# Kernel optimization log

Hardware: AMD Instinct MI355X
Metric: run time of the kernel (lower is better)

The kernel has to match this reference:

```python
import jax, jax.numpy as jnp
import numpy as np

NUM_HEADS = 16


def setup_inputs() -> dict:
    key = jax.random.key(0)
    ks = jax.random.split(key, 4)
    B, S, D = 2, 2048, 1024
    scale = 1.0 / np.sqrt(D)
    x = jax.random.normal(ks[0], (B, S, D), dtype=jnp.float32)
    Wq = jax.random.normal(ks[1], (D, D), dtype=jnp.float32) * scale
    Wk = jax.random.normal(ks[2], (D, D), dtype=jnp.float32) * scale
    Wv = jax.random.normal(ks[3], (D, D), dtype=jnp.float32) * scale
    bq = jnp.zeros((D,), dtype=jnp.float32)
    bk = jnp.zeros((D,), dtype=jnp.float32)
    bv = jnp.zeros((D,), dtype=jnp.float32)
    return {"x": x, "Wq": Wq, "bq": bq, "Wk": Wk, "bk": bk, "Wv": Wv, "bv": bv}


def _split_heads(t, H):
    B, S, D = t.shape
    return t.reshape(B, S, H, D // H).transpose(0, 2, 1, 3)  # (B,H,S,depth)


def reference(x, Wq, bq, Wk, bk, Wv, bv):
    H = NUM_HEADS
    B, S, D = x.shape
    depth = D // H
    q = _split_heads(x @ Wq + bq, H)
    k = _split_heads(x @ Wk + bk, H)
    v = _split_heads(x @ Wv + bv, H)
    # causal mask: strictly-upper-triangular ones, added as finfo.min * mask
    mask = 1.0 - jnp.tril(jnp.ones((S, S), dtype=jnp.float32))
    scores = jnp.einsum("bhqd,bhkd->bhqk", q, k) / jnp.sqrt(jnp.float32(depth))
    scores = scores + jnp.float32(np.finfo(np.float32).min) * mask
    probs = jax.nn.softmax(scores, axis=-1)
    att = jnp.einsum("bhqk,bhkd->bhqd", probs, v)
    return att.transpose(0, 2, 1, 3).reshape(B, S, D)
```

## Files before the change

### kernel.cpp

```cpp
#include <hip/hip_runtime.h>
#include <hip/hip_bf16.h>

#define B_ 2
#define S_ 2048
#define D_ 1024
#define H_ 16
#define DH 64
#define M_ (B_*S_)
#define NT_ (S_/64)

using bf16x8 = __attribute__((ext_vector_type(8))) __bf16;
using f32x4  = __attribute__((ext_vector_type(4))) float;

__device__ __forceinline__ int swz(int row) { return ((row ^ (row >> 3)) & 7) << 3; }

__device__ __forceinline__ void glds16(const __bf16* g, __bf16* l) {
#if __has_builtin(__builtin_amdgcn_global_load_lds)
  __builtin_amdgcn_global_load_lds(
      (const __attribute__((address_space(1))) unsigned int*)g,
      (__attribute__((address_space(3))) unsigned int*)l, 16, 0, 0);
#else
  *(bf16x8*)l = *(const bf16x8*)g;
#endif
}

__global__ __launch_bounds__(256) void conv_x(const float* __restrict__ x,
                                              __bf16* __restrict__ xb) {
  int idx = blockIdx.x * 256 + threadIdx.x;
  int m = idx >> 7, k = (idx & 127) * 8;
  float4 a = *(const float4*)&x[(size_t)m * D_ + k];
  float4 b = *(const float4*)&x[(size_t)m * D_ + k + 4];
  bf16x8 o;
  o[0]=(__bf16)a.x; o[1]=(__bf16)a.y; o[2]=(__bf16)a.z; o[3]=(__bf16)a.w;
  o[4]=(__bf16)b.x; o[5]=(__bf16)b.y; o[6]=(__bf16)b.z; o[7]=(__bf16)b.w;
  *(bf16x8*)&xb[(size_t)m * D_ + (k & ~63) + ((k & 63) ^ swz(m))] = o;
}

__global__ __launch_bounds__(256) void conv_w(const float* __restrict__ Wq,
                                              const float* __restrict__ Wk,
                                              const float* __restrict__ Wv,
                                              __bf16* __restrict__ wt) {
  int z = blockIdx.z;
  const float* __restrict__ W = (z == 0) ? Wq : (z == 1) ? Wk : Wv;
  __bf16* __restrict__ Wt = wt + (size_t)z * D_ * D_;
  __shared__ __bf16 Lt[64 * 66];
  int tid = threadIdx.x;
  int k0 = blockIdx.x * 64, n0 = blockIdx.y * 64;
  #pragma unroll
  for (int i = 0; i < 4; ++i) {
    int f4 = i * 256 + tid;
    int r = f4 >> 4, c4 = (f4 & 15) * 4;
    float4 v = *(const float4*)&W[(size_t)(k0 + r) * D_ + n0 + c4];
    Lt[(c4 + 0) * 66 + r] = (__bf16)v.x;
    Lt[(c4 + 1) * 66 + r] = (__bf16)v.y;
    Lt[(c4 + 2) * 66 + r] = (__bf16)v.z;
    Lt[(c4 + 3) * 66 + r] = (__bf16)v.w;
  }
  __syncthreads();
  #pragma unroll
  for (int i = 0; i < 2; ++i) {
    int idx = i * 256 + tid;
    int n = idx >> 3, kc = (idx & 7) * 8;
    int nf = n0 + n;
    bf16x8 o;
    #pragma unroll
    for (int j = 0; j < 8; ++j) o[j] = Lt[n * 66 + kc + j];
    *(bf16x8*)&Wt[(size_t)nf * D_ + k0 + (kc ^ swz(nf))] = o;
  }
}

#define BM 256
#define BN 256
#define BK 64
#define NKT (D_/BK)

__global__ __launch_bounds__(512, 2) void qkv_gemm(
    const __bf16* __restrict__ xb, const __bf16* __restrict__ wt,
    const float* __restrict__ bq, const float* __restrict__ bk,
    const float* __restrict__ bv, __bf16* __restrict__ qkv) {
  int z = blockIdx.z;
  const __bf16* __restrict__ Wt = wt + (size_t)z * D_ * D_;
  const float* __restrict__ bias = (z == 0) ? bq : (z == 1) ? bk : bv;
  __bf16* __restrict__ out = qkv + (size_t)z * M_ * D_;
  const float scale = (z == 0) ? 0.125f : 1.0f;

  __shared__ __bf16 Al[2][BM * BK];
  __shared__ __bf16 Bl[2][BM * BK];

  int tid = threadIdx.x, lane = tid & 63, w = tid >> 6;
  int m0 = blockIdx.y * BM, n0 = blockIdx.x * BN;
  int wr = (w >> 2) * 128;
  int wc = (w & 3) * 64;

  f32x4 acc[8][4] = {};

#define STAGE(buf, kt)                                                        \
  {                                                                           \
    int k0 = (kt) * BK;                                                       \
    _Pragma("unroll")                                                         \
    for (int r = 0; r < 4; ++r) {                                             \
      int e = (r * 512 + tid) * 8;                                            \
      int row = e >> 6, col = e & 63;                                         \
      glds16(&xb[(size_t)(m0 + row) * D_ + k0 + col], &Al[buf][e]);           \
      glds16(&Wt[(size_t)(n0 + row) * D_ + k0 + col], &Bl[buf][e]);           \
    }                                                                         \
  }

  STAGE(0, 0);
  __syncthreads();

  int cur = 0;
  for (int kt = 0; kt < NKT; ++kt) {
    if (kt + 1 < NKT) STAGE(cur ^ 1, kt + 1);
    #pragma unroll
    for (int kk = 0; kk < 2; ++kk) {
      bf16x8 af[8], bfr[4];
      #pragma unroll
      for (int mi = 0; mi < 8; ++mi) {
        int row = wr + mi * 16 + (lane & 15);
        af[mi] = *(const bf16x8*)&Al[cur][row * 64 +
                 ((kk * 32 + (lane >> 4) * 8) ^ swz(row))];
      }
      #pragma unroll
      for (int ni = 0; ni < 4; ++ni) {
        int col = wc + ni * 16 + (lane & 15);
        bfr[ni] = *(const bf16x8*)&Bl[cur][col * 64 +
                  ((kk * 32 + (lane >> 4) * 8) ^ swz(col))];
      }
      #pragma unroll
      for (int mi = 0; mi < 8; ++mi)
        #pragma unroll
        for (int ni = 0; ni < 4; ++ni)
          acc[mi][ni] = __builtin_amdgcn_mfma_f32_16x16x32_bf16(
              af[mi], bfr[ni], acc[mi][ni], 0, 0, 0);
    }
    __syncthreads();
    cur ^= 1;
  }
#undef STAGE

  #pragma unroll
  for (int mi = 0; mi < 8; ++mi) {
    #pragma unroll
    for (int ni = 0; ni < 4; ++ni) {
      int col = n0 + wc + ni * 16 + (lane & 15);
      int h = col >> 6, dh = col & 63;
      float bv_ = bias[col];
      #pragma unroll
      for (int r = 0; r < 4; ++r) {
        int row = m0 + wr + mi * 16 + (lane >> 4) * 4 + r;
        int b = row >> 11, s = row & 2047;
        out[((size_t)(b * H_ + h) * S_ + s) * DH + dh] =
            (__bf16)((acc[mi][ni][r] + bv_) * scale);
      }
    }
  }
}

__device__ __forceinline__ void attn_tile(
    const bf16x8* aq, f32x4* accO, float* mrow, float* lrow,
    const __bf16* __restrict__ Kl, const __bf16* __restrict__ Vt,
    __bf16* __restrict__ Plw, int lane, int kv0, int qbase, int diag) {
  f32x4 sf[4];
  __builtin_amdgcn_s_setprio(1);
  #pragma unroll
  for (int f = 0; f < 4; ++f) {
    f32x4 zz = {};
    int col = f * 16 + (lane & 15);
    int sc = swz(col);
    #pragma unroll
    for (int kk = 0; kk < 2; ++kk) {
      bf16x8 bk = *(const bf16x8*)&Kl[col * 64 + ((kk * 32 + (lane >> 4) * 8) ^ sc)];
      zz = __builtin_amdgcn_mfma_f32_16x16x32_bf16(aq[kk], bk, zz, 0, 0, 0);
    }
    sf[f] = zz;
  }
  __builtin_amdgcn_s_setprio(0);

  if (diag) {
    #pragma unroll
    for (int f = 0; f < 4; ++f) {
      int kvg = kv0 + f * 16 + (lane & 15);
      #pragma unroll
      for (int r = 0; r < 4; ++r) {
        int qg = qbase + (lane >> 4) * 4 + r;
        if (kvg > qg) sf[f][r] = -1e30f;
      }
    }
  }

  float alpha[4];
  #pragma unroll
  for (int r = 0; r < 4; ++r) {
    float mx = fmaxf(fmaxf(sf[0][r], sf[1][r]), fmaxf(sf[2][r], sf[3][r]));
    #pragma unroll
    for (int off = 8; off >= 1; off >>= 1)
      mx = fmaxf(mx, __shfl_xor(mx, off, 64));
    float mnew = fmaxf(mrow[r], mx);
    alpha[r] = __expf(mrow[r] - mnew);
    mrow[r] = mnew;
    float rs = 0.f;
    #pragma unroll
    for (int f = 0; f < 4; ++f) {
      float p = __expf(sf[f][r] - mnew);
      sf[f][r] = p;
      rs += p;
    }
    #pragma unroll
    for (int off = 8; off >= 1; off >>= 1)
      rs += __shfl_xor(rs, off, 64);
    lrow[r] = lrow[r] * alpha[r] + rs;
  }

  #pragma unroll
  for (int f = 0; f < 4; ++f)
    #pragma unroll
    for (int r = 0; r < 4; ++r) {
      int row = (lane >> 4) * 4 + r;
      Plw[row * 64 + ((f * 16 + (lane & 15)) ^ swz(row))] = (__bf16)sf[f][r];
    }

  #pragma unroll
  for (int f = 0; f < 4; ++f)
    #pragma unroll
    for (int r = 0; r < 4; ++r)
      accO[f][r] *= alpha[r];

  __builtin_amdgcn_s_setprio(1);
  #pragma unroll
  for (int kk = 0; kk < 2; ++kk) {
    int prow = lane & 15;
    bf16x8 pa = *(const bf16x8*)&Plw[prow * 64 + ((kk * 32 + (lane >> 4) * 8) ^ swz(prow))];
    #pragma unroll
    for (int f = 0; f < 4; ++f) {
      int vrow = f * 16 + (lane & 15);
      bf16x8 vb = *(const bf16x8*)&Vt[vrow * 64 + ((kk * 32 + (lane >> 4) * 8) ^ swz(vrow))];
      accO[f] = __builtin_amdgcn_mfma_f32_16x16x32_bf16(pa, vb, accO[f], 0, 0, 0);
    }
  }
  __builtin_amdgcn_s_setprio(0);
}

__device__ __forceinline__ void attn_out(
    const f32x4* accO, const float* lrow, float* __restrict__ out,
    int b, int h, int qbase, int lane) {
  #pragma unroll
  for (int f = 0; f < 4; ++f) {
    int dh = f * 16 + (lane & 15);
    #pragma unroll
    for (int r = 0; r < 4; ++r) {
      int qg = qbase + (lane >> 4) * 4 + r;
      out[((size_t)(b * S_ + qg)) * D_ + h * DH + dh] = accO[f][r] / lrow[r];
    }
  }
}

__global__ __launch_bounds__(256) void attn(
    const __bf16* __restrict__ Q, const __bf16* __restrict__ K,
    const __bf16* __restrict__ V, float* __restrict__ out) {
  __shared__ __bf16 Kl[64 * 64];
  __shared__ __bf16 Vt[64 * 64];
  __shared__ __bf16 Pl[4][16 * 64];

  int tid = threadIdx.x, lane = tid & 63, w = tid >> 6;
  int bx = blockIdx.x, h = blockIdx.y, b = blockIdx.z;
  int qA0 = bx * 64, qB0 = (NT_ - 1 - bx) * 64;
  size_t base = ((size_t)(b * H_ + h)) * S_ * DH;
  const __bf16* __restrict__ Qg = Q + base;
  const __bf16* __restrict__ Kg = K + base;
  const __bf16* __restrict__ Vg = V + base;

  bf16x8 aqA[2], aqB[2];
  int qra = qA0 + w * 16 + (lane & 15), qrb = qB0 + w * 16 + (lane & 15);
  #pragma unroll
  for (int kk = 0; kk < 2; ++kk) {
    aqA[kk] = *(const bf16x8*)&Qg[(size_t)qra * DH + kk * 32 + (lane >> 4) * 8];
    aqB[kk] = *(const bf16x8*)&Qg[(size_t)qrb * DH + kk * 32 + (lane >> 4) * 8];
  }

  f32x4 accA[4] = {}, accB[4] = {};
  float mA[4], lA[4], mB[4], lB[4];
  #pragma unroll
  for (int r = 0; r < 4; ++r) { mA[r] = mB[r] = -1e30f; lA[r] = lB[r] = 0.f; }

  const int ktA = bx, ktB = NT_ - 1 - bx;
  for (int kt = 0; kt <= ktB; ++kt) {
    int kv0 = kt * 64;
    #pragma unroll
    for (int i = 0; i < 2; ++i) {
      int e = (i * 256 + tid) * 8;
      int kv = e >> 6, d0 = e & 63;
      bf16x8 k8 = *(const bf16x8*)&Kg[(size_t)(kv0 + kv) * DH + d0];
      *(bf16x8*)&Kl[kv * 64 + (d0 ^ swz(kv))] = k8;
      bf16x8 v8 = *(const bf16x8*)&Vg[(size_t)(kv0 + kv) * DH + d0];
      #pragma unroll
      for (int j = 0; j < 8; ++j) {
        int row = d0 + j;
        Vt[row * 64 + (kv ^ swz(row))] = v8[j];
      }
    }
    __syncthreads();

    attn_tile(aqB, accB, mB, lB, Kl, Vt, Pl[w], lane, kv0, qB0 + w * 16, kt == ktB);
    if (kt <= ktA)
      attn_tile(aqA, accA, mA, lA, Kl, Vt, Pl[w], lane, kv0, qA0 + w * 16, kt == ktA);
    __syncthreads();
  }

  attn_out(accA, lA, out, b, h, qA0 + w * 16, lane);
  attn_out(accB, lB, out, b, h, qB0 + w * 16, lane);
}

extern "C" void kernel_launch(void* const* d_in, const int* in_sizes, int n_in,
                              void* d_out, int out_size, void* d_ws, size_t ws_size,
                              hipStream_t stream) {
  const float* x  = (const float*)d_in[0];
  const float* Wq = (const float*)d_in[1];
  const float* bq = (const float*)d_in[2];
  const float* Wk = (const float*)d_in[3];
  const float* bk = (const float*)d_in[4];
  const float* Wv = (const float*)d_in[5];
  const float* bv = (const float*)d_in[6];
  float* out = (float*)d_out;

  __bf16* xb  = (__bf16*)d_ws;
  __bf16* wt  = xb + (size_t)M_ * D_;
  __bf16* qkv = wt + (size_t)3 * D_ * D_;
  __bf16* wsq = qkv;
  __bf16* wsk = qkv + (size_t)M_ * D_;
  __bf16* wsv = qkv + (size_t)2 * M_ * D_;

  conv_x<<<(M_ * (D_ / 8)) / 256, 256, 0, stream>>>(x, xb);
  conv_w<<<dim3(D_ / 64, D_ / 64, 3), 256, 0, stream>>>(Wq, Wk, Wv, wt);
  qkv_gemm<<<dim3(D_ / BN, M_ / BM, 3), 512, 0, stream>>>(xb, wt, bq, bk, bv, qkv);
  attn<<<dim3(NT_ / 2, H_, B_), 256, 0, stream>>>(wsq, wsk, wsv, out);
}
```

Before: 198.9 us.

## Pre-transpose V, register-prefetch K/V tiles, and compute transposed scores in attention

Adds a separate kernel that transposes V into a per-head (DH x S) layout in reused workspace, so the attention kernel can stage V with vector stores instead of scalar transposing stores. The attention loop now prefetches the next K/V tile into registers while computing the current one. QK^T is computed transposed so each lane owns one query row, which cuts the softmax shuffles and holds m/l as scalars. Launch bounds change too: the GEMM drops its min-blocks hint and attention asks for 4 blocks per CU. The cost is an extra launch and extra register pressure from the prefetch buffers.

```diff
diff --git a/kernel.cpp b/kernel.cpp
--- a/kernel.cpp
+++ b/kernel.cpp
@@ -74,7 +74,7 @@
 #define BK 64
 #define NKT (D_/BK)
 
-__global__ __launch_bounds__(512, 2) void qkv_gemm(
+__global__ __launch_bounds__(512) void qkv_gemm(
     const __bf16* __restrict__ xb, const __bf16* __restrict__ wt,
     const float* __restrict__ bq, const float* __restrict__ bk,
     const float* __restrict__ bv, __bf16* __restrict__ qkv) {
@@ -157,107 +157,138 @@
   }
 }
 
-__device__ __forceinline__ void attn_tile(
-    const bf16x8* aq, f32x4* accO, float* mrow, float* lrow,
+__global__ __launch_bounds__(256) void vtrans(const __bf16* __restrict__ v,
+                                              __bf16* __restrict__ vt) {
+  __shared__ __bf16 Lt[64 * 64];
+  int tid = threadIdx.x;
+  int s0 = blockIdx.x * 64;
+  int h = blockIdx.y, b = blockIdx.z;
+  const __bf16* __restrict__ src = v + ((size_t)(b * H_ + h)) * S_ * DH;
+  __bf16* __restrict__ dst = vt + ((size_t)(b * H_ + h)) * DH * S_;
+  #pragma unroll
+  for (int i = 0; i < 2; ++i) {
+    int e = (i * 256 + tid) * 8;
+    int s = e >> 6, d0 = e & 63;
+    bf16x8 r = *(const bf16x8*)&src[(size_t)(s0 + s) * DH + d0];
+    #pragma unroll
+    for (int j = 0; j < 8; ++j) {
+      int d = d0 + j;
+      Lt[d * 64 + (s ^ swz(d))] = r[j];
+    }
+  }
+  __syncthreads();
+  #pragma unroll
+  for (int i = 0; i < 2; ++i) {
+    int e = (i * 256 + tid) * 8;
+    int d = e >> 6, sc = e & 63;
+    bf16x8 o = *(const bf16x8*)&Lt[d * 64 + (sc ^ swz(d))];
+    *(bf16x8*)&dst[(size_t)d * S_ + s0 + sc] = o;
+  }
+}
+
+__device__ __forceinline__ void attn_tile_sw(
+    const bf16x8* aq, f32x4* accO, float& m_reg, float& l_reg,
     const __bf16* __restrict__ Kl, const __bf16* __restrict__ Vt,
-    __bf16* __restrict__ Plw, int lane, int kv0, int qbase, int diag) {
-  f32x4 sf[4];
+    __bf16* __restrict__ Plw, int lane, int kv0, int qbase, bool diag) {
+  const int g = lane >> 4;
+  const int ql = lane & 15;
+  f32x4 sfT[4];
   __builtin_amdgcn_s_setprio(1);
   #pragma unroll
   for (int f = 0; f < 4; ++f) {
     f32x4 zz = {};
-    int col = f * 16 + (lane & 15);
-    int sc = swz(col);
+    int row = f * 16 + ql;
+    int sr = swz(row);
     #pragma unroll
     for (int kk = 0; kk < 2; ++kk) {
-      bf16x8 bk = *(const bf16x8*)&Kl[col * 64 + ((kk * 32 + (lane >> 4) * 8) ^ sc)];
-      zz = __builtin_amdgcn_mfma_f32_16x16x32_bf16(aq[kk], bk, zz, 0, 0, 0);
-    }
-    sf[f] = zz;
+      bf16x8 ka = *(const bf16x8*)&Kl[row * 64 + ((kk * 32 + g * 8) ^ sr)];
+      zz = __builtin_amdgcn_mfma_f32_16x16x32_bf16(ka, aq[kk], zz, 0, 0, 0);
+    }
+    sfT[f] = zz;
   }
   __builtin_amdgcn_s_setprio(0);
 
   if (diag) {
+    int qg = qbase + ql;
+    #pragma unroll
+    for (int f = 0; f < 4; ++f)
+      #pragma unroll
+      for (int r = 0; r < 4; ++r)
+        if (kv0 + f * 16 + g * 4 + r > qg) sfT[f][r] = -1e30f;
+  }
+
+  float mx = sfT[0][0];
+  #pragma unroll
+  for (int f = 0; f < 4; ++f)
+    #pragma unroll
+    for (int r = 0; r < 4; ++r) mx = fmaxf(mx, sfT[f][r]);
+  mx = fmaxf(mx, __shfl_xor(mx, 16, 64));
+  mx = fmaxf(mx, __shfl_xor(mx, 32, 64));
+  float mnew = fmaxf(m_reg, mx);
+  float alpha = __expf(m_reg - mnew);
+  m_reg = mnew;
+  float rs = 0.f;
+  #pragma unroll
+  for (int f = 0; f < 4; ++f)
+    #pragma unroll
+    for (int r = 0; r < 4; ++r) {
+      float p = __expf(sfT[f][r] - mnew);
+      sfT[f][r] = p;
+      rs += p;
+    }
+  rs += __shfl_xor(rs, 16, 64);
+  rs += __shfl_xor(rs, 32, 64);
+  l_reg = l_reg * alpha + rs;
+
+  const int key = (ql & 7) << 3;
+  #pragma unroll
+  for (int f = 0; f < 4; ++f)
+    #pragma unroll
+    for (int r = 0; r < 4; ++r)
+      Plw[ql * 64 + ((f * 16 + g * 4 + r) ^ key)] = (__bf16)sfT[f][r];
+
+  float ab[4];
+  #pragma unroll
+  for (int r = 0; r < 4; ++r) ab[r] = __shfl(alpha, g * 4 + r, 16);
+  #pragma unroll
+  for (int f = 0; f < 4; ++f)
+    #pragma unroll
+    for (int r = 0; r < 4; ++r) accO[f][r] *= ab[r];
+
+  __builtin_amdgcn_s_setprio(1);
+  #pragma unroll
+  for (int kk = 0; kk < 2; ++kk) {
+    bf16x8 pa = *(const bf16x8*)&Plw[ql * 64 + ((kk * 32 + g * 8) ^ key)];
     #pragma unroll
     for (int f = 0; f < 4; ++f) {
-      int kvg = kv0 + f * 16 + (lane & 15);
-      #pragma unroll
-      for (int r = 0; r < 4; ++r) {
-        int qg = qbase + (lane >> 4) * 4 + r;
-        if (kvg > qg) sf[f][r] = -1e30f;
-      }
-    }
-  }
-
-  float alpha[4];
-  #pragma unroll
-  for (int r = 0; r < 4; ++r) {
-    float mx = fmaxf(fmaxf(sf[0][r], sf[1][r]), fmaxf(sf[2][r], sf[3][r]));
-    #pragma unroll
-    for (int off = 8; off >= 1; off >>= 1)
-      mx = fmaxf(mx, __shfl_xor(mx, off, 64));
-    float mnew = fmaxf(mrow[r], mx);
-    alpha[r] = __expf(mrow[r] - mnew);
-    mrow[r] = mnew;
-    float rs = 0.f;
-    #pragma unroll
-    for (int f = 0; f < 4; ++f) {
-      float p = __expf(sf[f][r] - mnew);
-      sf[f][r] = p;
-      rs += p;
-    }
-    #pragma unroll
-    for (int off = 8; off >= 1; off >>= 1)
-      rs += __shfl_xor(rs, off, 64);
-    lrow[r] = lrow[r] * alpha[r] + rs;
-  }
-
-  #pragma unroll
-  for (int f = 0; f < 4; ++f)
-    #pragma unroll
-    for (int r = 0; r < 4; ++r) {
-      int row = (lane >> 4) * 4 + r;
-      Plw[row * 64 + ((f * 16 + (lane & 15)) ^ swz(row))] = (__bf16)sf[f][r];
-    }
-
-  #pragma unroll
-  for (int f = 0; f < 4; ++f)
-    #pragma unroll
-    for (int r = 0; r < 4; ++r)
-      accO[f][r] *= alpha[r];
-
-  __builtin_amdgcn_s_setprio(1);
-  #pragma unroll
-  for (int kk = 0; kk < 2; ++kk) {
-    int prow = lane & 15;
-    bf16x8 pa = *(const bf16x8*)&Plw[prow * 64 + ((kk * 32 + (lane >> 4) * 8) ^ swz(prow))];
-    #pragma unroll
-    for (int f = 0; f < 4; ++f) {
-      int vrow = f * 16 + (lane & 15);
-      bf16x8 vb = *(const bf16x8*)&Vt[vrow * 64 + ((kk * 32 + (lane >> 4) * 8) ^ swz(vrow))];
+      int vrow = f * 16 + ql;
+      bf16x8 vb = *(const bf16x8*)&Vt[vrow * 64 + ((kk * 32 + g * 8) ^ swz(vrow))];
       accO[f] = __builtin_amdgcn_mfma_f32_16x16x32_bf16(pa, vb, accO[f], 0, 0, 0);
     }
   }
   __builtin_amdgcn_s_setprio(0);
 }
 
-__device__ __forceinline__ void attn_out(
-    const f32x4* accO, const float* lrow, float* __restrict__ out,
+__device__ __forceinline__ void attn_out_sw(
+    const f32x4* accO, float l_reg, float* __restrict__ out,
     int b, int h, int qbase, int lane) {
+  float lr[4];
+  #pragma unroll
+  for (int r = 0; r < 4; ++r) lr[r] = __shfl(l_reg, (lane >> 4) * 4 + r, 16);
   #pragma unroll
   for (int f = 0; f < 4; ++f) {
     int dh = f * 16 + (lane & 15);
     #pragma unroll
     for (int r = 0; r < 4; ++r) {
       int qg = qbase + (lane >> 4) * 4 + r;
-      out[((size_t)(b * S_ + qg)) * D_ + h * DH + dh] = accO[f][r] / lrow[r];
-    }
-  }
-}
-
-__global__ __launch_bounds__(256) void attn(
+      out[((size_t)(b * S_ + qg)) * D_ + h * DH + dh] = accO[f][r] / lr[r];
+    }
+  }
+}
+
+__global__ __launch_bounds__(256, 4) void attn(
     const __bf16* __restrict__ Q, const __bf16* __restrict__ K,
-    const __bf16* __restrict__ V, float* __restrict__ out) {
+    const __bf16* __restrict__ VT, float* __restrict__ out) {
   __shared__ __bf16 Kl[64 * 64];
   __shared__ __bf16 Vt[64 * 64];
   __shared__ __bf16 Pl[4][16 * 64];
@@ -268,7 +299,7 @@
   size_t base = ((size_t)(b * H_ + h)) * S_ * DH;
   const __bf16* __restrict__ Qg = Q + base;
   const __bf16* __restrict__ Kg = K + base;
-  const __bf16* __restrict__ Vg = V + base;
+  const __bf16* __restrict__ VTg = VT + base;
 
   bf16x8 aqA[2], aqB[2];
   int qra = qA0 + w * 16 + (lane & 15), qrb = qB0 + w * 16 + (lane & 15);
@@ -279,36 +310,49 @@
   }
 
   f32x4 accA[4] = {}, accB[4] = {};
-  float mA[4], lA[4], mB[4], lB[4];
-  #pragma unroll
-  for (int r = 0; r < 4; ++r) { mA[r] = mB[r] = -1e30f; lA[r] = lB[r] = 0.f; }
+  float mA = -1e30f, lA = 0.f, mB = -1e30f, lB = 0.f;
 
   const int ktA = bx, ktB = NT_ - 1 - bx;
+
+  bf16x8 kreg[2], vreg[2];
+  #pragma unroll
+  for (int i = 0; i < 2; ++i) {
+    int e = (i * 256 + tid) * 8;
+    kreg[i] = *(const bf16x8*)&Kg[(size_t)(e >> 6) * DH + (e & 63)];
+    vreg[i] = *(const bf16x8*)&VTg[(size_t)(e >> 6) * S_ + (e & 63)];
+  }
+
   for (int kt = 0; kt <= ktB; ++kt) {
     int kv0 = kt * 64;
     #pragma unroll
     for (int i = 0; i < 2; ++i) {
       int e = (i * 256 + tid) * 8;
-      int kv = e >> 6, d0 = e & 63;
-      bf16x8 k8 = *(const bf16x8*)&Kg[(size_t)(kv0 + kv) * DH + d0];
-      *(bf16x8*)&Kl[kv * 64 + (d0 ^ swz(kv))] = k8;
-      bf16x8 v8 = *(const bf16x8*)&Vg[(size_t)(kv0 + kv) * DH + d0];
-      #pragma unroll
-      for (int j = 0; j < 8; ++j) {
-        int row = d0 + j;
-        Vt[row * 64 + (kv ^ swz(row))] = v8[j];
+      int rrow = e >> 6, cc = e & 63;
+      *(bf16x8*)&Kl[rrow * 64 + (cc ^ swz(rrow))] = kreg[i];
+      *(bf16x8*)&Vt[rrow * 64 + (cc ^ swz(rrow))] = vreg[i];
+    }
+    __syncthreads();
+
+    if (kt < ktB) {
+      int kvn = kv0 + 64;
+      #pragma unroll
+      for (int i = 0; i < 2; ++i) {
+        int e = (i * 256 + tid) * 8;
+        kreg[i] = *(const bf16x8*)&Kg[(size_t)(kvn + (e >> 6)) * DH + (e & 63)];
+        vreg[i] = *(const bf16x8*)&VTg[(size_t)(e >> 6) * S_ + kvn + (e & 63)];
       }
     }
+
+    attn_tile_sw(aqB, accB, mB, lB, Kl, Vt, Pl[w], lane, kv0, qB0 + w * 16,
+                 kt == ktB);
+    if (kt <= ktA)
+      attn_tile_sw(aqA, accA, mA, lA, Kl, Vt, Pl[w], lane, kv0, qA0 + w * 16,
+                   kt == ktA);
     __syncthreads();
-
-    attn_tile(aqB, accB, mB, lB, Kl, Vt, Pl[w], lane, kv0, qB0 + w * 16, kt == ktB);
-    if (kt <= ktA)
-      attn_tile(aqA, accA, mA, lA, Kl, Vt, Pl[w], lane, kv0, qA0 + w * 16, kt == ktA);
-    __syncthreads();
-  }
-
-  attn_out(accA, lA, out, b, h, qA0 + w * 16, lane);
-  attn_out(accB, lB, out, b, h, qB0 + w * 16, lane);
+  }
+
+  attn_out_sw(accA, lA, out, b, h, qA0 + w * 16, lane);
+  attn_out_sw(accB, lB, out, b, h, qB0 + w * 16, lane);
 }
 
 extern "C" void kernel_launch(void* const* d_in, const int* in_sizes, int n_in,
@@ -329,9 +373,11 @@
   __bf16* wsq = qkv;
   __bf16* wsk = qkv + (size_t)M_ * D_;
   __bf16* wsv = qkv + (size_t)2 * M_ * D_;
+  __bf16* vtg = xb;
 
   conv_x<<<(M_ * (D_ / 8)) / 256, 256, 0, stream>>>(x, xb);
   conv_w<<<dim3(D_ / 64, D_ / 64, 3), 256, 0, stream>>>(Wq, Wk, Wv, wt);
   qkv_gemm<<<dim3(D_ / BN, M_ / BM, 3), 512, 0, stream>>>(xb, wt, bq, bk, bv, qkv);
-  attn<<<dim3(NT_ / 2, H_, B_), 256, 0, stream>>>(wsq, wsk, wsv, out);
-}
+  vtrans<<<dim3(S_ / 64, H_, B_), 256, 0, stream>>>(wsv, vtg);
+  attn<<<dim3(NT_ / 2, H_, B_), 256, 0, stream>>>(wsq, wsk, vtg, out);
+}
```

New measurement: 251.1 us. 26.3% more time.
